# Kernel tuning notes

Hardware: AMD Instinct MI355X
Metric: run time of the kernel (lower is better)

The kernel has to match this reference:

```python
import jax, jax.numpy as jnp
import numpy as np

COMMITMENT_COST = 0.25
N_EMBED = 1024
EMB_DIM = 256

def setup_inputs() -> dict:
    key = jax.random.key(0)
    k1, k2 = jax.random.split(key)
    z = jax.random.normal(k1, (32, EMB_DIM, 32, 32), dtype=jnp.float32)
    # embedding.weight.data.uniform_(-1/n_embed, 1/n_embed)
    embedding = jax.random.uniform(k2, (N_EMBED, EMB_DIM), dtype=jnp.float32,
                                   minval=-1.0 / N_EMBED, maxval=1.0 / N_EMBED)
    return {"z": z, "embedding": embedding}

def reference(z, embedding):
    # NCHW -> NHWC
    zp = jnp.transpose(z, (0, 2, 3, 1))            # [B,H,W,D]
    in_shape = zp.shape
    flat = zp.reshape(-1, in_shape[-1])            # [N,D]
    # squared L2 distances (argmin equivalent to p=2 cdist argmin)
    d2 = (jnp.sum(flat * flat, axis=1, keepdims=True)
          - 2.0 * (flat @ embedding.T)
          + jnp.sum(embedding * embedding, axis=1))  # [N,K]
    idx = jnp.argmin(d2, axis=1)                   # [N]
    # one-hot @ codebook == direct gather
    z_quant = embedding[idx].reshape(in_shape)     # [B,H,W,D]
    codebook_loss = jnp.mean((z_quant - jax.lax.stop_gradient(zp)) ** 2)
    commitment_loss = jnp.mean((zp - jax.lax.stop_gradient(z_quant)) ** 2)
    loss = codebook_loss + COMMITMENT_COST * commitment_loss
    # straight-through estimator
    z_st = zp + jax.lax.stop_gradient(z_quant - zp)
    z_st = jnp.transpose(z_st, (0, 3, 1, 2))       # NHWC -> NCHW
    return (z_st, loss, codebook_loss, commitment_loss)
```

## Files before the change

kernel.cpp:

```cpp
#include <hip/hip_runtime.h>
#include <hip/hip_bf16.h>
#include <stdint.h>


typedef short v8s __attribute__((ext_vector_type(8)));
typedef float v4f __attribute__((ext_vector_type(4)));

__device__ inline unsigned short f2bf(float f) {
    uint32_t u = __float_as_uint(f);
    return (unsigned short)((u + 0x7fffu + ((u >> 16) & 1u)) >> 16);
}

__global__ __launch_bounds__(256) void k_prep_e(const float* __restrict__ E,
                                                v8s* __restrict__ Esw,
                                                float* __restrict__ nE,
                                                float* __restrict__ accum) {
    __shared__ float Ef[16][264];
    int q = blockIdx.x, tid = threadIdx.x;
    const float4* Ein = (const float4*)(E + ((size_t)q << 12));
#pragma unroll
    for (int i = 0; i < 4; i++) {
        int f4 = i * 256 + tid;
        int row = f4 >> 6, c4 = (f4 & 63) << 2;
        *(float4*)&Ef[row][c4] = Ein[f4];
    }
    __syncthreads();
    {
        int c = tid >> 4, l = tid & 15;
        float s = 0.f;
#pragma unroll
        for (int j = 0; j < 16; j++) { float v = Ef[c][l + 16 * j]; s += v * v; }
#pragma unroll
        for (int off = 1; off < 16; off <<= 1) s += __shfl_xor(s, off);
        if (l == 0) nE[q * 16 + c] = 0.5f * s;
    }
#pragma unroll
    for (int i = 0; i < 2; i++) {
        int u = tid + i * 256;
        int um = u & 15, ug = (u >> 4) & 3, udc = (u >> 6) & 7;
        int d0 = udc * 32 + ug * 8;
        union { v8s v; unsigned short s[8]; } pk;
#pragma unroll
        for (int e = 0; e < 8; e++) pk.s[e] = f2bf(Ef[um][d0 + e]);
        Esw[((size_t)q << 9) + u] = pk.v;
    }
    if (q == 0 && tid == 0) accum[0] = 0.f;
}

__global__ __launch_bounds__(512) void k_main(
        const v8s* __restrict__ Esw,
        const float* __restrict__ nE,
        const float* __restrict__ z,
        const float* __restrict__ E,
        float* __restrict__ out,
        float* __restrict__ accum) {
    __shared__ union {
        v8s    B[2][2048];
        float4 Eg4[2048];
    } S;
    __shared__ float nEl[1024];
    __shared__ int   idxLds[128];
    __shared__ float w8[8];

    int tid = threadIdx.x;
    int lane = tid & 63, w = tid >> 6;
    int g = lane >> 4, m = lane & 15;
    int R0 = blockIdx.x << 7;
    int b = R0 >> 10, hw0 = R0 & 1023;

    {
        int q = tid & 31, dblk = tid >> 5;
        const float* zp = z + ((size_t)b << 18) + hw0 + (q << 2);
#pragma unroll
        for (int s = 0; s < 2; s++) {
            float4 L[8];
#pragma unroll
            for (int j = 0; j < 8; j++)
                L[j] = *(const float4*)(zp + (size_t)(((dblk << 4) + (s << 3) + j) << 10));
            const float* Lf = (const float*)L;
            int slot = (dblk << 1) + s;
#pragma unroll
            for (int c = 0; c < 4; c++) {
                union { v8s v; unsigned short u[8]; } pk;
#pragma unroll
                for (int j = 0; j < 8; j++) pk.u[j] = f2bf(Lf[j * 4 + c]);
                int row = (q << 2) + c;
                int sw = slot ^ ((row ^ (row >> 2)) & 7);
                *(v8s*)((char*)&S + (row << 9) + (sw << 4)) = pk.v;
            }
        }
    }
#pragma unroll
    for (int i = 0; i < 2; i++) nEl[tid + i * 512] = nE[tid + i * 512];
    __syncthreads();

    v8s a[8];
    float nrm = 0.f;
    {
        int row = (w << 4) + m;
        int f = (row ^ (row >> 2)) & 7;
#pragma unroll
        for (int dc = 0; dc < 8; dc++) {
            int sw = ((dc << 2) + g) ^ f;
            a[dc] = *(const v8s*)((const char*)&S + (row << 9) + (sw << 4));
        }
#pragma unroll
        for (int dc = 0; dc < 8; dc++) {
            union { v8s v; unsigned short u[8]; } un; un.v = a[dc];
#pragma unroll
            for (int j = 0; j < 8; j++) {
                float v = __uint_as_float((uint32_t)un.u[j] << 16);
                nrm = fmaf(v, v, nrm);
            }
        }
        nrm += __shfl_xor(nrm, 16);
        nrm += __shfl_xor(nrm, 32);
    }
    __syncthreads();

#define STAGE(ch, buf)                                                        \
    {                                                                         \
        _Pragma("unroll")                                                     \
        for (int j = 0; j < 4; j++) {                                         \
            __builtin_amdgcn_global_load_lds(                                 \
                (const __attribute__((address_space(1))) void*)               \
                    (Esw + ((size_t)(ch) << 11) + (j << 9) + (w << 6) + lane),\
                (__attribute__((address_space(3))) void*)                     \
                    &S.B[buf][(j << 9) + (w << 6)],                           \
                16, 0, 0);                                                    \
        }                                                                     \
    }

    float best[4]; int bidx[4];
#pragma unroll
    for (int r = 0; r < 4; r++) { best[r] = 3.4e38f; bidx[r] = 0; }

    STAGE(0, 0);
#pragma unroll 1
    for (int ct = 0; ct < 16; ct++) {
        int cur = ct & 1;
        __syncthreads();
        if (ct < 15) STAGE(ct + 1, cur ^ 1);
        float ne[4];
#pragma unroll
        for (int t = 0; t < 4; t++) ne[t] = nEl[(ct << 6) + t * 16 + m];
        v4f acc[4];
#pragma unroll
        for (int t = 0; t < 4; t++) acc[t] = (v4f){0.f, 0.f, 0.f, 0.f};
#pragma unroll
        for (int dc = 0; dc < 8; dc++) {
#pragma unroll
            for (int t = 0; t < 4; t++) {
                v8s bf = S.B[cur][t * 512 + dc * 64 + g * 16 + m];
                acc[t] = __builtin_amdgcn_mfma_f32_16x16x32_bf16(a[dc], bf, acc[t], 0, 0, 0);
            }
        }
#pragma unroll
        for (int t = 0; t < 4; t++) {
            int code = (ct << 6) + t * 16 + m;
#pragma unroll
            for (int r = 0; r < 4; r++) {
                float s0 = ne[t] - acc[t][r];
                if (s0 < best[r]) { best[r] = s0; bidx[r] = code; }
            }
        }
    }

    float lsum = 0.f;
#pragma unroll
    for (int r = 0; r < 4; r++) {
        uint32_t sb = __float_as_uint(best[r]);
        sb = (sb & 0x80000000u) ? ~sb : (sb | 0x80000000u);
        unsigned long long pk = ((unsigned long long)sb << 32) | (uint32_t)bidx[r];
#pragma unroll
        for (int off = 1; off < 16; off <<= 1) {
            unsigned long long o = __shfl_xor(pk, off);
            if (o < pk) pk = o;
        }
        float rn = __shfl(nrm, (g << 2) + r);
        if (m == 0) {
            idxLds[w * 16 + g * 4 + r] = (int)(pk & 0xffffffffu);
            uint32_t t = (uint32_t)(pk >> 32);
            float sw = __uint_as_float((t & 0x80000000u) ? (t & 0x7fffffffu) : ~t);
            lsum += 2.0f * sw + rn;
        }
    }
    __syncthreads();

    float* ob = out + ((size_t)b << 18);
    int hwl = tid & 31, dq0 = tid >> 5;
#pragma unroll 1
    for (int ph = 0; ph < 4; ph++) {
#pragma unroll
        for (int i = 0; i < 4; i++) {
            int row = w + (i << 3);
            int k = idxLds[(ph << 5) + row];
            float4 v = ((const float4*)(E + ((size_t)k << 8)))[lane];
            S.Eg4[(row << 6) + (lane ^ row)] = v;
        }
        __syncthreads();
        int hwp = hw0 + (ph << 5) + hwl;
#pragma unroll
        for (int i = 0; i < 4; i++) {
            int dq = dq0 + (i << 4);
            float4 ev = S.Eg4[(hwl << 6) + (dq ^ hwl)];
            size_t o = ((size_t)dq << 12) + hwp;
            ob[o] = ev.x; ob[o + 1024] = ev.y; ob[o + 2048] = ev.z; ob[o + 3072] = ev.w;
        }
        __syncthreads();
    }
#pragma unroll
    for (int off = 1; off < 64; off <<= 1) lsum += __shfl_xor(lsum, off);
    if (lane == 0) w8[w] = lsum;
    __syncthreads();
    if (tid == 0) {
        float s = 0.f;
#pragma unroll
        for (int i = 0; i < 8; i++) s += w8[i];
        atomicAdd(accum, s);
    }
#undef STAGE
}

__global__ void k_loss(const float* __restrict__ accum, float* __restrict__ out) {
    if (threadIdx.x == 0) {
        float s = accum[0] * (1.0f / 8388608.0f);
        out[8388608] = 1.25f * s;
        out[8388609] = s;
        out[8388610] = s;
    }
}

extern "C" void kernel_launch(void* const* d_in, const int* in_sizes, int n_in,
                              void* d_out, int out_size, void* d_ws, size_t ws_size,
                              hipStream_t stream) {
    const float* z = (const float*)d_in[0];
    const float* E = (const float*)d_in[1];
    char* ws = (char*)d_ws;
    v8s*   Esw   = (v8s*)(ws);
    float* nE    = (float*)(ws + 524288);
    float* accum = (float*)(ws + 528384);
    float* out = (float*)d_out;

    hipLaunchKernelGGL(k_prep_e, dim3(64),  dim3(256), 0, stream, E, Esw, nE, accum);
    hipLaunchKernelGGL(k_main,   dim3(256), dim3(512), 0, stream,
                       Esw, nE, z, E, out, accum);
    hipLaunchKernelGGL(k_loss,   dim3(1),   dim3(64),  0, stream, accum, out);
}
```

Measured before the change: 121.3 us.

## Retile MFMA work as 2x2 per wave and fold loss kernel into main

Each wave now computes two 16-row tiles against two 16-code tiles, so every B fragment loaded from LDS feeds two MFMAs. Previously each wave did one row tile against four code tiles. The argmin is split across two wave halves and merged through shared memory, which adds a sync and some LDS traffic. The separate loss kernel is removed: the last block, found with an atomic counter, writes the final losses, saving one launch at the cost of a threadfence and an extra atomic.

Result: no change. 123.6 us (+1.9%).

```diff
diff --git a/kernel.cpp b/kernel.cpp
--- a/kernel.cpp
+++ b/kernel.cpp
@@ -14,7 +14,8 @@
 __global__ __launch_bounds__(256) void k_prep_e(const float* __restrict__ E,
                                                 v8s* __restrict__ Esw,
                                                 float* __restrict__ nE,
-                                                float* __restrict__ accum) {
+                                                float* __restrict__ accum,
+                                                unsigned* __restrict__ done) {
     __shared__ float Ef[16][264];
     int q = blockIdx.x, tid = threadIdx.x;
     const float4* Ein = (const float4*)(E + ((size_t)q << 12));
@@ -44,7 +45,7 @@
         for (int e = 0; e < 8; e++) pk.s[e] = f2bf(Ef[um][d0 + e]);
         Esw[((size_t)q << 9) + u] = pk.v;
     }
-    if (q == 0 && tid == 0) accum[0] = 0.f;
+    if (q == 0 && tid == 0) { accum[0] = 0.f; done[0] = 0u; }
 }
 
 __global__ __launch_bounds__(512) void k_main(
@@ -53,18 +54,22 @@
         const float* __restrict__ z,
         const float* __restrict__ E,
         float* __restrict__ out,
-        float* __restrict__ accum) {
+        float* __restrict__ accum,
+        unsigned* __restrict__ done) {
     __shared__ union {
         v8s    B[2][2048];
         float4 Eg4[2048];
     } S;
     __shared__ float nEl[1024];
+    __shared__ unsigned long long pairLds[128][2];
+    __shared__ float nrmLds[128];
     __shared__ int   idxLds[128];
-    __shared__ float w8[8];
+    __shared__ float w8[2];
 
     int tid = threadIdx.x;
     int lane = tid & 63, w = tid >> 6;
     int g = lane >> 4, m = lane & 15;
+    int rg = w & 3, h = w >> 2;
     int R0 = blockIdx.x << 7;
     int b = R0 >> 10, hw0 = R0 & 1023;
 
@@ -94,27 +99,31 @@
     for (int i = 0; i < 2; i++) nEl[tid + i * 512] = nE[tid + i * 512];
     __syncthreads();
 
-    v8s a[8];
-    float nrm = 0.f;
+    v8s a[2][8];
     {
-        int row = (w << 4) + m;
-        int f = (row ^ (row >> 2)) & 7;
-#pragma unroll
-        for (int dc = 0; dc < 8; dc++) {
-            int sw = ((dc << 2) + g) ^ f;
-            a[dc] = *(const v8s*)((const char*)&S + (row << 9) + (sw << 4));
-        }
-#pragma unroll
-        for (int dc = 0; dc < 8; dc++) {
-            union { v8s v; unsigned short u[8]; } un; un.v = a[dc];
-#pragma unroll
-            for (int j = 0; j < 8; j++) {
-                float v = __uint_as_float((uint32_t)un.u[j] << 16);
-                nrm = fmaf(v, v, nrm);
-            }
-        }
-        nrm += __shfl_xor(nrm, 16);
-        nrm += __shfl_xor(nrm, 32);
+#pragma unroll
+        for (int mt = 0; mt < 2; mt++) {
+            int row = (rg << 5) + (mt << 4) + m;
+            int f = (row ^ (row >> 2)) & 7;
+#pragma unroll
+            for (int dc = 0; dc < 8; dc++) {
+                int sw = ((dc << 2) + g) ^ f;
+                a[mt][dc] = *(const v8s*)((const char*)&S + (row << 9) + (sw << 4));
+            }
+            float nrm = 0.f;
+#pragma unroll
+            for (int dc = 0; dc < 8; dc++) {
+                union { v8s v; unsigned short u[8]; } un; un.v = a[mt][dc];
+#pragma unroll
+                for (int j = 0; j < 8; j++) {
+                    float v = __uint_as_float((uint32_t)un.u[j] << 16);
+                    nrm = fmaf(v, v, nrm);
+                }
+            }
+            nrm += __shfl_xor(nrm, 16);
+            nrm += __shfl_xor(nrm, 32);
+            if (h == 0 && g == 0) nrmLds[row] = nrm;
+        }
     }
     __syncthreads();
 
@@ -131,9 +140,11 @@
         }                                                                     \
     }
 
-    float best[4]; int bidx[4];
-#pragma unroll
-    for (int r = 0; r < 4; r++) { best[r] = 3.4e38f; bidx[r] = 0; }
+    float best[2][4]; int bidx[2][4];
+#pragma unroll
+    for (int mt = 0; mt < 2; mt++)
+#pragma unroll
+        for (int r = 0; r < 4; r++) { best[mt][r] = 3.4e38f; bidx[mt][r] = 0; }
 
     STAGE(0, 0);
 #pragma unroll 1
@@ -141,50 +152,65 @@
         int cur = ct & 1;
         __syncthreads();
         if (ct < 15) STAGE(ct + 1, cur ^ 1);
-        float ne[4];
-#pragma unroll
-        for (int t = 0; t < 4; t++) ne[t] = nEl[(ct << 6) + t * 16 + m];
-        v4f acc[4];
-#pragma unroll
-        for (int t = 0; t < 4; t++) acc[t] = (v4f){0.f, 0.f, 0.f, 0.f};
+        float ne[2];
+#pragma unroll
+        for (int t = 0; t < 2; t++) ne[t] = nEl[(ct << 6) + (h << 5) + (t << 4) + m];
+        v4f acc[2][2];
+#pragma unroll
+        for (int mt = 0; mt < 2; mt++)
+#pragma unroll
+            for (int t = 0; t < 2; t++) acc[mt][t] = (v4f){0.f, 0.f, 0.f, 0.f};
 #pragma unroll
         for (int dc = 0; dc < 8; dc++) {
 #pragma unroll
-            for (int t = 0; t < 4; t++) {
-                v8s bf = S.B[cur][t * 512 + dc * 64 + g * 16 + m];
-                acc[t] = __builtin_amdgcn_mfma_f32_16x16x32_bf16(a[dc], bf, acc[t], 0, 0, 0);
-            }
-        }
-#pragma unroll
-        for (int t = 0; t < 4; t++) {
-            int code = (ct << 6) + t * 16 + m;
-#pragma unroll
-            for (int r = 0; r < 4; r++) {
-                float s0 = ne[t] - acc[t][r];
-                if (s0 < best[r]) { best[r] = s0; bidx[r] = code; }
-            }
-        }
-    }
+            for (int t = 0; t < 2; t++) {
+                v8s bf = S.B[cur][((h << 1) + t) * 512 + dc * 64 + g * 16 + m];
+                acc[0][t] = __builtin_amdgcn_mfma_f32_16x16x32_bf16(a[0][dc], bf, acc[0][t], 0, 0, 0);
+                acc[1][t] = __builtin_amdgcn_mfma_f32_16x16x32_bf16(a[1][dc], bf, acc[1][t], 0, 0, 0);
+            }
+        }
+#pragma unroll
+        for (int t = 0; t < 2; t++) {
+            int code = (ct << 6) + (h << 5) + (t << 4) + m;
+#pragma unroll
+            for (int mt = 0; mt < 2; mt++)
+#pragma unroll
+                for (int r = 0; r < 4; r++) {
+                    float s0 = ne[t] - acc[mt][t][r];
+                    if (s0 < best[mt][r]) { best[mt][r] = s0; bidx[mt][r] = code; }
+                }
+        }
+    }
+
+#pragma unroll
+    for (int mt = 0; mt < 2; mt++)
+#pragma unroll
+        for (int r = 0; r < 4; r++) {
+            uint32_t sb = __float_as_uint(best[mt][r]);
+            sb = (sb & 0x80000000u) ? ~sb : (sb | 0x80000000u);
+            unsigned long long pk = ((unsigned long long)sb << 32) | (uint32_t)bidx[mt][r];
+#pragma unroll
+            for (int off = 1; off < 16; off <<= 1) {
+                unsigned long long o = __shfl_xor(pk, off);
+                if (o < pk) pk = o;
+            }
+            if (m == 0)
+                pairLds[(rg << 5) + (mt << 4) + (g << 2) + r][h] = pk;
+        }
+    __syncthreads();
 
     float lsum = 0.f;
-#pragma unroll
-    for (int r = 0; r < 4; r++) {
-        uint32_t sb = __float_as_uint(best[r]);
-        sb = (sb & 0x80000000u) ? ~sb : (sb | 0x80000000u);
-        unsigned long long pk = ((unsigned long long)sb << 32) | (uint32_t)bidx[r];
-#pragma unroll
-        for (int off = 1; off < 16; off <<= 1) {
-            unsigned long long o = __shfl_xor(pk, off);
-            if (o < pk) pk = o;
-        }
-        float rn = __shfl(nrm, (g << 2) + r);
-        if (m == 0) {
-            idxLds[w * 16 + g * 4 + r] = (int)(pk & 0xffffffffu);
-            uint32_t t = (uint32_t)(pk >> 32);
-            float sw = __uint_as_float((t & 0x80000000u) ? (t & 0x7fffffffu) : ~t);
-            lsum += 2.0f * sw + rn;
-        }
-    }
+    if (tid < 128) {
+        unsigned long long p0 = pairLds[tid][0], p1 = pairLds[tid][1];
+        unsigned long long pk = p1 < p0 ? p1 : p0;
+        idxLds[tid] = (int)(pk & 0xffffffffu);
+        uint32_t t = (uint32_t)(pk >> 32);
+        float sc = __uint_as_float((t & 0x80000000u) ? (t & 0x7fffffffu) : ~t);
+        lsum = 2.0f * sc + nrmLds[tid];
+    }
+#pragma unroll
+    for (int off = 1; off < 64; off <<= 1) lsum += __shfl_xor(lsum, off);
+    if (lane == 0 && w < 2) w8[w] = lsum;
     __syncthreads();
 
     float* ob = out + ((size_t)b << 18);
@@ -209,26 +235,19 @@
         }
         __syncthreads();
     }
-#pragma unroll
-    for (int off = 1; off < 64; off <<= 1) lsum += __shfl_xor(lsum, off);
-    if (lane == 0) w8[w] = lsum;
-    __syncthreads();
+
     if (tid == 0) {
-        float s = 0.f;
-#pragma unroll
-        for (int i = 0; i < 8; i++) s += w8[i];
-        atomicAdd(accum, s);
+        atomicAdd(accum, w8[0] + w8[1]);
+        __threadfence();
+        unsigned old = atomicAdd(done, 1u);
+        if (old == 255u) {
+            float s = atomicAdd(accum, 0.f) * (1.0f / 8388608.0f);
+            out[8388608] = 1.25f * s;
+            out[8388609] = s;
+            out[8388610] = s;
+        }
     }
 #undef STAGE
-}
-
-__global__ void k_loss(const float* __restrict__ accum, float* __restrict__ out) {
-    if (threadIdx.x == 0) {
-        float s = accum[0] * (1.0f / 8388608.0f);
-        out[8388608] = 1.25f * s;
-        out[8388609] = s;
-        out[8388610] = s;
-    }
 }
 
 extern "C" void kernel_launch(void* const* d_in, const int* in_sizes, int n_in,
@@ -237,13 +256,13 @@
     const float* z = (const float*)d_in[0];
     const float* E = (const float*)d_in[1];
     char* ws = (char*)d_ws;
-    v8s*   Esw   = (v8s*)(ws);
-    float* nE    = (float*)(ws + 524288);
-    float* accum = (float*)(ws + 528384);
+    v8s*      Esw   = (v8s*)(ws);
+    float*    nE    = (float*)(ws + 524288);
+    float*    accum = (float*)(ws + 528384);
+    unsigned* done  = (unsigned*)(ws + 528388);
     float* out = (float*)d_out;
 
-    hipLaunchKernelGGL(k_prep_e, dim3(64),  dim3(256), 0, stream, E, Esw, nE, accum);
+    hipLaunchKernelGGL(k_prep_e, dim3(64),  dim3(256), 0, stream, E, Esw, nE, accum, done);
     hipLaunchKernelGGL(k_main,   dim3(256), dim3(512), 0, stream,
-                       Esw, nE, z, E, out, accum);
-    hipLaunchKernelGGL(k_loss,   dim3(1),   dim3(64),  0, stream, accum, out);
-}
+                       Esw, nE, z, E, out, accum, done);
+}
```

## Double codebook chunk size and fuse loss finalization into main kernel

Applied to the files above, without the earlier changes.

Codebook tiles staged into LDS grow from 64 to 128 codes per iteration, which halves the loop trips and barriers and gives each wave 8 independent MFMA accumulators. The separate loss kernel is removed: the last block to finish, detected with an atomic counter, writes the final loss values, saving one launch. Row norms move to LDS and the per-block loss reduction is hoisted ahead of the output writes. The cost is higher LDS use (64KB B buffers) and more accumulator registers, which may lower occupancy.

Measured after the change: 116.9 us. -3.6%, faster.

```diff
diff --git a/kernel.cpp b/kernel.cpp
--- a/kernel.cpp
+++ b/kernel.cpp
@@ -14,7 +14,8 @@
 __global__ __launch_bounds__(256) void k_prep_e(const float* __restrict__ E,
                                                 v8s* __restrict__ Esw,
                                                 float* __restrict__ nE,
-                                                float* __restrict__ accum) {
+                                                float* __restrict__ accum,
+                                                unsigned* __restrict__ done) {
     __shared__ float Ef[16][264];
     int q = blockIdx.x, tid = threadIdx.x;
     const float4* Ein = (const float4*)(E + ((size_t)q << 12));
@@ -44,7 +45,7 @@
         for (int e = 0; e < 8; e++) pk.s[e] = f2bf(Ef[um][d0 + e]);
         Esw[((size_t)q << 9) + u] = pk.v;
     }
-    if (q == 0 && tid == 0) accum[0] = 0.f;
+    if (q == 0 && tid == 0) { accum[0] = 0.f; done[0] = 0u; }
 }
 
 __global__ __launch_bounds__(512) void k_main(
@@ -53,12 +54,14 @@
         const float* __restrict__ z,
         const float* __restrict__ E,
         float* __restrict__ out,
-        float* __restrict__ accum) {
+        float* __restrict__ accum,
+        unsigned* __restrict__ done) {
     __shared__ union {
-        v8s    B[2][2048];
+        v8s    B[2][4096];
         float4 Eg4[2048];
     } S;
     __shared__ float nEl[1024];
+    __shared__ float nrmLds[128];
     __shared__ int   idxLds[128];
     __shared__ float w8[8];
 
@@ -95,7 +98,6 @@
     __syncthreads();
 
     v8s a[8];
-    float nrm = 0.f;
     {
         int row = (w << 4) + m;
         int f = (row ^ (row >> 2)) & 7;
@@ -104,6 +106,7 @@
             int sw = ((dc << 2) + g) ^ f;
             a[dc] = *(const v8s*)((const char*)&S + (row << 9) + (sw << 4));
         }
+        float nrm = 0.f;
 #pragma unroll
         for (int dc = 0; dc < 8; dc++) {
             union { v8s v; unsigned short u[8]; } un; un.v = a[dc];
@@ -115,16 +118,17 @@
         }
         nrm += __shfl_xor(nrm, 16);
         nrm += __shfl_xor(nrm, 32);
+        if (g == 0) nrmLds[row] = nrm;
     }
     __syncthreads();
 
 #define STAGE(ch, buf)                                                        \
     {                                                                         \
         _Pragma("unroll")                                                     \
-        for (int j = 0; j < 4; j++) {                                         \
+        for (int j = 0; j < 8; j++) {                                         \
             __builtin_amdgcn_global_load_lds(                                 \
                 (const __attribute__((address_space(1))) void*)               \
-                    (Esw + ((size_t)(ch) << 11) + (j << 9) + (w << 6) + lane),\
+                    (Esw + ((size_t)(ch) << 12) + (j << 9) + (w << 6) + lane),\
                 (__attribute__((address_space(3))) void*)                     \
                     &S.B[buf][(j << 9) + (w << 6)],                           \
                 16, 0, 0);                                                    \
@@ -136,28 +140,28 @@
     for (int r = 0; r < 4; r++) { best[r] = 3.4e38f; bidx[r] = 0; }
 
     STAGE(0, 0);
-#pragma unroll 1
-    for (int ct = 0; ct < 16; ct++) {
+#pragma unroll 2
+    for (int ct = 0; ct < 8; ct++) {
         int cur = ct & 1;
         __syncthreads();
-        if (ct < 15) STAGE(ct + 1, cur ^ 1);
-        float ne[4];
-#pragma unroll
-        for (int t = 0; t < 4; t++) ne[t] = nEl[(ct << 6) + t * 16 + m];
-        v4f acc[4];
-#pragma unroll
-        for (int t = 0; t < 4; t++) acc[t] = (v4f){0.f, 0.f, 0.f, 0.f};
+        if (ct < 7) STAGE(ct + 1, cur ^ 1);
+        float ne[8];
+#pragma unroll
+        for (int t = 0; t < 8; t++) ne[t] = nEl[(ct << 7) + (t << 4) + m];
+        v4f acc[8];
+#pragma unroll
+        for (int t = 0; t < 8; t++) acc[t] = (v4f){0.f, 0.f, 0.f, 0.f};
 #pragma unroll
         for (int dc = 0; dc < 8; dc++) {
 #pragma unroll
-            for (int t = 0; t < 4; t++) {
+            for (int t = 0; t < 8; t++) {
                 v8s bf = S.B[cur][t * 512 + dc * 64 + g * 16 + m];
                 acc[t] = __builtin_amdgcn_mfma_f32_16x16x32_bf16(a[dc], bf, acc[t], 0, 0, 0);
             }
         }
 #pragma unroll
-        for (int t = 0; t < 4; t++) {
-            int code = (ct << 6) + t * 16 + m;
+        for (int t = 0; t < 8; t++) {
+            int code = (ct << 7) + (t << 4) + m;
 #pragma unroll
             for (int r = 0; r < 4; r++) {
                 float s0 = ne[t] - acc[t][r];
@@ -177,14 +181,17 @@
             unsigned long long o = __shfl_xor(pk, off);
             if (o < pk) pk = o;
         }
-        float rn = __shfl(nrm, (g << 2) + r);
+        int row = (w << 4) + (g << 2) + r;
         if (m == 0) {
-            idxLds[w * 16 + g * 4 + r] = (int)(pk & 0xffffffffu);
+            idxLds[row] = (int)(pk & 0xffffffffu);
             uint32_t t = (uint32_t)(pk >> 32);
             float sw = __uint_as_float((t & 0x80000000u) ? (t & 0x7fffffffu) : ~t);
-            lsum += 2.0f * sw + rn;
-        }
-    }
+            lsum += 2.0f * sw + nrmLds[row];
+        }
+    }
+#pragma unroll
+    for (int off = 1; off < 64; off <<= 1) lsum += __shfl_xor(lsum, off);
+    if (lane == 0) w8[w] = lsum;
     __syncthreads();
 
     float* ob = out + ((size_t)b << 18);
@@ -209,26 +216,22 @@
         }
         __syncthreads();
     }
-#pragma unroll
-    for (int off = 1; off < 64; off <<= 1) lsum += __shfl_xor(lsum, off);
-    if (lane == 0) w8[w] = lsum;
-    __syncthreads();
+
     if (tid == 0) {
-        float s = 0.f;
-#pragma unroll
-        for (int i = 0; i < 8; i++) s += w8[i];
-        atomicAdd(accum, s);
+        float s8 = 0.f;
+#pragma unroll
+        for (int i = 0; i < 8; i++) s8 += w8[i];
+        atomicAdd(accum, s8);
+        __threadfence();
+        unsigned old = atomicAdd(done, 1u);
+        if (old == 255u) {
+            float s = atomicAdd(accum, 0.f) * (1.0f / 8388608.0f);
+            out[8388608] = 1.25f * s;
+            out[8388609] = s;
+            out[8388610] = s;
+        }
     }
 #undef STAGE
-}
-
-__global__ void k_loss(const float* __restrict__ accum, float* __restrict__ out) {
-    if (threadIdx.x == 0) {
-        float s = accum[0] * (1.0f / 8388608.0f);
-        out[8388608] = 1.25f * s;
-        out[8388609] = s;
-        out[8388610] = s;
-    }
 }
 
 extern "C" void kernel_launch(void* const* d_in, const int* in_sizes, int n_in,
@@ -237,13 +240,13 @@
     const float* z = (const float*)d_in[0];
     const float* E = (const float*)d_in[1];
     char* ws = (char*)d_ws;
-    v8s*   Esw   = (v8s*)(ws);
-    float* nE    = (float*)(ws + 524288);
-    float* accum = (float*)(ws + 528384);
+    v8s*      Esw   = (v8s*)(ws);
+    float*    nE    = (float*)(ws + 524288);
+    float*    accum = (float*)(ws + 528384);
+    unsigned* done  = (unsigned*)(ws + 528388);
     float* out = (float*)d_out;
 
-    hipLaunchKernelGGL(k_prep_e, dim3(64),  dim3(256), 0, stream, E, Esw, nE, accum);
+    hipLaunchKernelGGL(k_prep_e, dim3(64),  dim3(256), 0, stream, E, Esw, nE, accum, done);
     hipLaunchKernelGGL(k_main,   dim3(256), dim3(512), 0, stream,
-                       Esw, nE, z, E, out, accum);
-    hipLaunchKernelGGL(k_loss,   dim3(1),   dim3(64),  0, stream, accum, out);
-}
+                       Esw, nE, z, E, out, accum, done);
+}
```
